# Kernel optimization log

Hardware: AMD Instinct MI355X
Metric: run time of the kernel (lower is better)

Reference implementation:

```python
import jax, jax.numpy as jnp
import numpy as np
import math

N_HEAD = 16
STRIDE = 128
C = 8


def _sparse_causal_mask(q_len, k_len):
    # Mirrors LingLongAttention._sparse_causal_mask (static, host-side numpy).
    cols = np.arange(k_len)
    rows = np.arange(k_len)[:, None]
    strided = (cols % STRIDE) >= (STRIDE - C)          # last C cols of each stride block
    local = (cols[None, :] // STRIDE) == (rows // STRIDE)  # same stride block as query
    causal = cols[None, :] <= rows
    layout = (strided[None, :] | local) & causal       # [k_len, k_len]
    return jnp.asarray(layout[k_len - q_len:])         # [q_len, k_len]


def setup_inputs() -> dict:
    key = jax.random.key(0)
    k1, k2, k3 = jax.random.split(key, 3)
    B, S, E = 2, 2048, 1024
    return {
        "hidden_states": jax.random.normal(k1, (B, S, E), dtype=jnp.float32),
        "W_attn": jax.random.normal(k2, (E, 3 * E), dtype=jnp.float32) * 0.02,
        "b_attn": jnp.zeros((3 * E,), dtype=jnp.float32),
        "W_proj": jax.random.normal(k3, (E, E), dtype=jnp.float32) * 0.02,
        "b_proj": jnp.zeros((E,), dtype=jnp.float32),
    }


def reference(hidden_states, W_attn, b_attn, W_proj, b_proj):
    B, S, E = hidden_states.shape
    H = N_HEAD
    D = E // H
    # Conv1D: x @ W + b, then split into q,k,v
    qkv = hidden_states @ W_attn + b_attn                 # [B,S,3E]
    q, k, v = jnp.split(qkv, 3, axis=-1)
    split = lambda t: t.reshape(B, S, H, D).transpose(0, 2, 1, 3)  # [B,H,S,D]
    q, k, v = split(q), split(k), split(v)
    scale = jnp.asarray(1.0 / math.sqrt(D), dtype=q.dtype)
    scores = jnp.einsum("bhqd,bhkd->bhqk", q, k) * scale  # [B,H,S,S]
    mask = _sparse_causal_mask(S, S)[None, None]          # [1,1,S,S]
    mask_value = jnp.asarray(jnp.finfo(scores.dtype).min, dtype=scores.dtype)
    scores = jnp.where(mask, scores, mask_value)
    attn = jax.nn.softmax(scores, axis=-1)
    out = jnp.einsum("bhqk,bhkd->bhqd", attn, v)          # [B,H,S,D]
    out = out.transpose(0, 2, 1, 3).reshape(B, S, E)      # merge heads
    return out @ W_proj + b_proj
```

## Files before the change

### kernel.cpp

```cpp
#include <hip/hip_runtime.h>
#include <hip/hip_bf16.h>
#include <stdint.h>

typedef unsigned short u16;
typedef uint32_t u32;
typedef short s16x8 __attribute__((ext_vector_type(8)));
typedef float f32x4 __attribute__((ext_vector_type(4)));

#define SDIM 2048
#define EDIM 1024

static __device__ __forceinline__ float b2f(u16 v) {
    union { float f; u32 u; } c; c.u = ((u32)v) << 16; return c.f;
}
static __device__ __forceinline__ u16 f2b(float f) {
    union { float f; u32 u; } c; c.f = f;
    u32 u = c.u;
    u32 r = (u + 0x7FFFu + ((u >> 16) & 1u)) >> 16;
    return (u16)r;
}
static __device__ __forceinline__ void gll16(const u16* g, u16* l) {
    __builtin_amdgcn_global_load_lds(
        (const __attribute__((address_space(1))) void*)g,
        (__attribute__((address_space(3))) void*)l, 16, 0, 0);
}

static __device__ __forceinline__ int sniff_bf16(const u16* __restrict__ x) {
    u16 v = x[(threadIdx.x & 63) * 2];
    int e = (v >> 7) & 0xFF;
    unsigned long long m = __ballot(e >= 90 && e <= 144);
    return __popcll(m) >= 48;
}

__global__ __launch_bounds__(256) void k_prep(
    const void* __restrict__ X, const void* __restrict__ Wa,
    const void* __restrict__ Wp, u16* __restrict__ Xb,
    u16* __restrict__ WtA, u16* __restrict__ WtP) {
    int f = sniff_bf16((const u16*)X);
    int z = blockIdx.z;
    int t = threadIdx.x;
    if (z == 2) {
        if (f) return;
        const float* s = (const float*)X;
        int bid = blockIdx.y * 48 + blockIdx.x;
        for (int c = bid; c < 2048; c += 768) {
            long i = ((long)c * 256 + t) * 8;
            u16 o[8];
            for (int j = 0; j < 8; ++j) o[j] = f2b(s[i + j]);
            *(uint4*)&Xb[i] = *(uint4*)o;
        }
        return;
    }
    if (z == 1 && blockIdx.x >= 16) return;
    const void* src = z ? Wp : Wa;
    u16* dst = z ? WtP : WtA;
    int Nsrc = z ? 1024 : 3072;
    int n0 = blockIdx.x * 64, k0 = blockIdx.y * 64;
    __shared__ u16 L[64 * 72];
    int r = t >> 2, c0 = (t & 3) * 16;
    u16 val[16];
    if (f) {
        const u16* s = (const u16*)src + (size_t)(k0 + r) * Nsrc + n0 + c0;
        *(uint4*)&val[0] = *(const uint4*)s;
        *(uint4*)&val[8] = *(const uint4*)(s + 8);
    } else {
        const float* s = (const float*)src + (size_t)(k0 + r) * Nsrc + n0 + c0;
        for (int j = 0; j < 16; ++j) val[j] = f2b(s[j]);
    }
    for (int j = 0; j < 16; ++j) L[(c0 + j) * 72 + r] = val[j];
    __syncthreads();
    uint4 o0 = *(const uint4*)&L[r * 72 + c0];
    uint4 o1 = *(const uint4*)&L[r * 72 + c0 + 8];
    u16* d = dst + (size_t)(n0 + r) * 1024 + k0 + c0;
    *(uint4*)d = o0;
    *(uint4*)(d + 8) = o1;
}

__global__ __launch_bounds__(256) void k_gemm1(
    const u16* __restrict__ Xraw, const u16* __restrict__ Xb,
    const u16* __restrict__ Bt, const void* __restrict__ bias,
    u16* __restrict__ C) {
    const int K = 1024;
    __shared__ u16 As[2][4096];
    __shared__ u16 Bs[2][4096];
    int f = sniff_bf16(Xraw);
    const u16* A = f ? Xraw : Xb;
    int t = threadIdx.x, wave = t >> 6, lane = t & 63;
    int m0 = blockIdx.y * 128, n0 = blockIdx.x * 128;
    int wm = (wave >> 1) * 64, wn = (wave & 1) * 64;
    int lm = lane & 15, lk = (lane >> 4) * 8;
    int sr = t >> 2, sc = (t & 3) * 8;
    const u16* Ap = A + (size_t)(m0 + sr) * K + sc;
    const u16* Bp = Bt + (size_t)(n0 + sr) * K + sc;
    int wo = wave * 512;

    f32x4 acc[4][4];
    f32x4 z = {0.f, 0.f, 0.f, 0.f};
    for (int mi = 0; mi < 4; ++mi)
        for (int ni = 0; ni < 4; ++ni) acc[mi][ni] = z;

    gll16(Ap, &As[0][wo]);
    gll16(Ap + (size_t)64 * K, &As[0][wo + 2048]);
    gll16(Bp, &Bs[0][wo]);
    gll16(Bp + (size_t)64 * K, &Bs[0][wo + 2048]);
    __syncthreads();

    for (int it = 0; it < 32; ++it) {
        int cur = it & 1;
        if (it < 31) {
            int kn = (it + 1) * 32;
            gll16(Ap + kn, &As[cur ^ 1][wo]);
            gll16(Ap + (size_t)64 * K + kn, &As[cur ^ 1][wo + 2048]);
            gll16(Bp + kn, &Bs[cur ^ 1][wo]);
            gll16(Bp + (size_t)64 * K + kn, &Bs[cur ^ 1][wo + 2048]);
        }
        s16x8 af[4], bfr[4];
        for (int mi = 0; mi < 4; ++mi)
            af[mi] = *(const s16x8*)&As[cur][(wm + mi * 16 + lm) * 32 + lk];
        for (int ni = 0; ni < 4; ++ni)
            bfr[ni] = *(const s16x8*)&Bs[cur][(wn + ni * 16 + lm) * 32 + lk];
        for (int mi = 0; mi < 4; ++mi)
            for (int ni = 0; ni < 4; ++ni)
                acc[mi][ni] = __builtin_amdgcn_mfma_f32_16x16x32_bf16(
                    af[mi], bfr[ni], acc[mi][ni], 0, 0, 0);
        __syncthreads();
    }

    int cn = lane & 15, cr = (lane >> 4) * 4;
    for (int ni = 0; ni < 4; ++ni) {
        int gn = n0 + wn + ni * 16 + cn;
        float bb = f ? b2f(((const u16*)bias)[gn]) : ((const float*)bias)[gn];
        int kind = gn >> 10, rem = gn & 1023;
        int h = rem >> 6, d = rem & 63;
        int hm = kind * 32 + h;
        for (int mi = 0; mi < 4; ++mi)
            for (int r = 0; r < 4; ++r) {
                int gm = m0 + wm + mi * 16 + cr + r;
                int b = gm >> 11, s = gm & 2047;
                size_t o = ((size_t)((hm + b * 16) * 2048 + s)) * 64 + d;
                C[o] = f2b(acc[mi][ni][r] + bb);
            }
    }
}

__global__ __launch_bounds__(256) void k_gemm2(
    const u16* __restrict__ Xraw, const u16* __restrict__ A,
    const u16* __restrict__ Bt, const void* __restrict__ bias,
    u16* __restrict__ Cb, float* __restrict__ Cf) {
    const int K = 1024, N = 1024;
    __shared__ u16 As[2][2048];
    __shared__ u16 Bs[2][4096];
    int f = sniff_bf16(Xraw);
    int t = threadIdx.x, wave = t >> 6, lane = t & 63;
    int m0 = blockIdx.y * 64, n0 = blockIdx.x * 128;
    int wm = (wave >> 1) * 32, wn = (wave & 1) * 64;
    int lm = lane & 15, lk = (lane >> 4) * 8;
    int sr = t >> 2, sc = (t & 3) * 8;
    const u16* Ap = A + (size_t)(m0 + sr) * K + sc;
    const u16* Bp = Bt + (size_t)(n0 + sr) * K + sc;
    int wo = wave * 512;

    f32x4 acc[2][4];
    f32x4 z = {0.f, 0.f, 0.f, 0.f};
    for (int mi = 0; mi < 2; ++mi)
        for (int ni = 0; ni < 4; ++ni) acc[mi][ni] = z;

    gll16(Ap, &As[0][wo]);
    gll16(Bp, &Bs[0][wo]);
    gll16(Bp + (size_t)64 * K, &Bs[0][wo + 2048]);
    __syncthreads();

    for (int it = 0; it < 32; ++it) {
        int cur = it & 1;
        if (it < 31) {
            int kn = (it + 1) * 32;
            gll16(Ap + kn, &As[cur ^ 1][wo]);
            gll16(Bp + kn, &Bs[cur ^ 1][wo]);
            gll16(Bp + (size_t)64 * K + kn, &Bs[cur ^ 1][wo + 2048]);
        }
        s16x8 af[2], bfr[4];
        for (int mi = 0; mi < 2; ++mi)
            af[mi] = *(const s16x8*)&As[cur][(wm + mi * 16 + lm) * 32 + lk];
        for (int ni = 0; ni < 4; ++ni)
            bfr[ni] = *(const s16x8*)&Bs[cur][(wn + ni * 16 + lm) * 32 + lk];
        for (int mi = 0; mi < 2; ++mi)
            for (int ni = 0; ni < 4; ++ni)
                acc[mi][ni] = __builtin_amdgcn_mfma_f32_16x16x32_bf16(
                    af[mi], bfr[ni], acc[mi][ni], 0, 0, 0);
        __syncthreads();
    }

    int store_f32 = (f == 0);
    int cn = lane & 15, cr = (lane >> 4) * 4;
    for (int ni = 0; ni < 4; ++ni) {
        int gn = n0 + wn + ni * 16 + cn;
        float bb = f ? b2f(((const u16*)bias)[gn]) : ((const float*)bias)[gn];
        for (int mi = 0; mi < 2; ++mi)
            for (int r = 0; r < 4; ++r) {
                int gm = m0 + wm + mi * 16 + cr + r;
                float v = acc[mi][ni][r] + bb;
                size_t o = (size_t)gm * N + gn;
                if (store_f32) Cf[o] = v;
                else           Cb[o] = f2b(v);
            }
    }
}

#define VP 264
#define PP 264
__global__ __launch_bounds__(256) void k_attn4(const u16* __restrict__ QKV,
                                               u16* __restrict__ AO) {
    int bx = blockIdx.x, h = blockIdx.y, b = blockIdx.z;
    int qb = bx >> 1, sb = bx & 1;
    int t = threadIdx.x, lane = t & 63, wave = t >> 6;
    int lm = lane & 15, q4 = lane >> 4;
    int nstr = qb << 3;
    int nk = nstr + (sb << 6) + 64;
    int r0 = (qb << 7) + (sb << 6);

    __shared__ char smem[79872];
    u16* Vts = (u16*)smem;
    u16* Qs  = (u16*)(smem + 33792);
    u16* Ks  = (u16*)(smem + 33792 + 9216);
    u16* Ps  = (u16*)(smem + 33792);

    int hm = b * 16 + h;
    const u16* qp = QKV + ((size_t)hm * 2048 + r0) * 64;
    const u16* kp = QKV + ((size_t)(32 + hm) * 2048) * 64;
    const u16* vp = QKV + ((size_t)(64 + hm) * 2048) * 64;

    for (int c = t; c < 512; c += 256) {
        int r = c >> 3, d0 = (c & 7) << 3;
        *(uint4*)&Qs[r * 72 + d0] = *(const uint4*)(qp + c * 8);
    }
    uint4 zz = {0u, 0u, 0u, 0u};
    for (int c = t; c < 2048; c += 256) {
        int i = c >> 3, d0 = (c & 7) << 3;
        uint4 kv = zz;
        if (i < nk) {
            int key = (i < nstr) ? (((i >> 3) << 7) + 120 + (i & 7))
                                 : ((qb << 7) + (i - nstr));
            kv = *(const uint4*)(kp + key * 64 + d0);
        }
        *(uint4*)&Ks[i * 72 + d0] = kv;
    }
    {
        int i0 = (t & 31) * 8, d0 = (t >> 5) * 8;
        u16 m8[8][8];
        for (int r = 0; r < 8; ++r) {
            int i = i0 + r;
            uint4 vv = zz;
            if (i < nk) {
                int key = (i < nstr) ? (((i >> 3) << 7) + 120 + (i & 7))
                                     : ((qb << 7) + (i - nstr));
                vv = *(const uint4*)(vp + key * 64 + d0);
            }
            *(uint4*)m8[r] = vv;
        }
        for (int j = 0; j < 8; ++j) {
            u16 o[8];
            for (int r = 0; r < 8; ++r) o[r] = m8[r][j];
            *(uint4*)&Vts[(d0 + j) * VP + i0] = *(uint4*)o;
        }
    }
    __syncthreads();

    f32x4 acc[16];
    f32x4 z4 = {0.f, 0.f, 0.f, 0.f};
    for (int ni = 0; ni < 16; ++ni) acc[ni] = z4;
    s16x8 af0 = *(const s16x8*)&Qs[(wave * 16 + lm) * 72 + q4 * 8];
    s16x8 af1 = *(const s16x8*)&Qs[(wave * 16 + lm) * 72 + 32 + q4 * 8];
    for (int ni = 0; ni < 16; ++ni) {
        s16x8 bf0 = *(const s16x8*)&Ks[(ni * 16 + lm) * 72 + q4 * 8];
        s16x8 bf1 = *(const s16x8*)&Ks[(ni * 16 + lm) * 72 + 32 + q4 * 8];
        acc[ni] = __builtin_amdgcn_mfma_f32_16x16x32_bf16(af0, bf0, acc[ni], 0, 0, 0);
        acc[ni] = __builtin_amdgcn_mfma_f32_16x16x32_bf16(af1, bf1, acc[ni], 0, 0, 0);
    }
    __syncthreads();

    float mx[4] = {-3e38f, -3e38f, -3e38f, -3e38f};
    for (int ni = 0; ni < 16; ++ni) {
        int i = ni * 16 + lm;
        for (int reg = 0; reg < 4; ++reg) {
            int rl = (sb << 6) + wave * 16 + q4 * 4 + reg;
            bool valid = (i < nstr) || ((i - nstr) <= rl);
            float v = valid ? acc[ni][reg] * 0.125f : -3e38f;
            acc[ni][reg] = v;
            mx[reg] = fmaxf(mx[reg], v);
        }
    }
    for (int reg = 0; reg < 4; ++reg)
        for (int off = 1; off < 16; off <<= 1)
            mx[reg] = fmaxf(mx[reg], __shfl_xor(mx[reg], off, 64));
    float sm[4] = {0.f, 0.f, 0.f, 0.f};
    for (int ni = 0; ni < 16; ++ni)
        for (int reg = 0; reg < 4; ++reg) {
            float e = __expf(acc[ni][reg] - mx[reg]);
            acc[ni][reg] = e;
            sm[reg] += e;
        }
    for (int reg = 0; reg < 4; ++reg)
        for (int off = 1; off < 16; off <<= 1)
            sm[reg] += __shfl_xor(sm[reg], off, 64);
    float inv[4];
    for (int reg = 0; reg < 4; ++reg) inv[reg] = 1.f / sm[reg];

    for (int ni = 0; ni < 16; ++ni) {
        int i = ni * 16 + lm;
        for (int reg = 0; reg < 4; ++reg)
            Ps[(wave * 16 + q4 * 4 + reg) * PP + i] = f2b(acc[ni][reg]);
    }
    __syncthreads();

    f32x4 acc2[4];
    for (int ni2 = 0; ni2 < 4; ++ni2) acc2[ni2] = z4;
    for (int k0 = 0; k0 < 256; k0 += 32) {
        s16x8 pf = *(const s16x8*)&Ps[(wave * 16 + lm) * PP + k0 + q4 * 8];
        for (int ni2 = 0; ni2 < 4; ++ni2) {
            s16x8 vf = *(const s16x8*)&Vts[(ni2 * 16 + lm) * VP + k0 + q4 * 8];
            acc2[ni2] = __builtin_amdgcn_mfma_f32_16x16x32_bf16(pf, vf, acc2[ni2], 0, 0, 0);
        }
    }
    int srow = r0 + wave * 16 + q4 * 4;
    for (int ni2 = 0; ni2 < 4; ++ni2)
        for (int reg = 0; reg < 4; ++reg) {
            size_t o = ((size_t)(b * SDIM + srow + reg)) * EDIM + h * 64 + ni2 * 16 + lm;
            AO[o] = f2b(acc2[ni2][reg] * inv[reg]);
        }
}

extern "C" void kernel_launch(void* const* d_in, const int* in_sizes, int n_in,
                              void* d_out, int out_size, void* d_ws, size_t ws_size,
                              hipStream_t stream) {
    const void* X  = d_in[0];
    const void* Wa = d_in[1];
    const void* ba = d_in[2];
    const void* Wp = d_in[3];
    const void* bp = d_in[4];

    char* w = (char*)d_ws;
    u16* Xb   = (u16*)(w);
    u16* WtA  = (u16*)(w + 8388608);
    u16* WtP  = (u16*)(w + 14680064);
    u16* QKVh = (u16*)(w + 16777216);
    u16* AO   = (u16*)(w + 41943040);

    k_prep<<<dim3(48, 16, 3), 256, 0, stream>>>(X, Wa, Wp, Xb, WtA, WtP);
    k_gemm1<<<dim3(24, 32), 256, 0, stream>>>((const u16*)X, Xb, WtA, ba, QKVh);
    k_attn4<<<dim3(32, 16, 2), 256, 0, stream>>>(QKVh, AO);
    k_gemm2<<<dim3(8, 64), 256, 0, stream>>>((const u16*)X, AO, WtP, bp,
                                             (u16*)d_out, (float*)d_out);
}
```

Measured before the change: 169.4 us.

## Deepen GEMM LDS pipeline with split-K stages and fine-grained vmcnt waits

Both projection GEMMs now keep two K=64 buffers, each split into two 32-wide chunks, and issue the next tile's loads chunk by chunk. Full __syncthreads barriers are replaced by explicit s_waitcnt vmcnt(N) plus s_barrier, so only the oldest chunk has to land before it is used. This keeps more global-to-LDS loads in flight across the MFMA work, at the cost of doubled LDS use and hand-tuned wait counts. The last iteration issues a redundant wraparound prefetch that is drained with vmcnt(0).

```diff
diff --git a/kernel.cpp b/kernel.cpp
--- a/kernel.cpp
+++ b/kernel.cpp
@@ -76,55 +76,68 @@
     *(uint4*)(d + 8) = o1;
 }
 
+#define G1_STAGE(bufi, kc, kt) do {                                          \
+    gll16(Ab + (kt) * 64 + (kc) * 32,             &As[bufi][kc][wave * 512]); \
+    gll16(Ab + (kt) * 64 + (kc) * 32 + 64 * 1024, &As[bufi][kc][wave * 512 + 2048]); \
+    gll16(Bb + (kt) * 64 + (kc) * 32,             &Bs[bufi][kc][wave * 512]); \
+    gll16(Bb + (kt) * 64 + (kc) * 32 + 64 * 1024, &Bs[bufi][kc][wave * 512 + 2048]); \
+} while (0)
+
 __global__ __launch_bounds__(256) void k_gemm1(
     const u16* __restrict__ Xraw, const u16* __restrict__ Xb,
     const u16* __restrict__ Bt, const void* __restrict__ bias,
     u16* __restrict__ C) {
     const int K = 1024;
-    __shared__ u16 As[2][4096];
-    __shared__ u16 Bs[2][4096];
+    __shared__ u16 As[2][2][4096];
+    __shared__ u16 Bs[2][2][4096];
     int f = sniff_bf16(Xraw);
     const u16* A = f ? Xraw : Xb;
     int t = threadIdx.x, wave = t >> 6, lane = t & 63;
     int m0 = blockIdx.y * 128, n0 = blockIdx.x * 128;
     int wm = (wave >> 1) * 64, wn = (wave & 1) * 64;
-    int lm = lane & 15, lk = (lane >> 4) * 8;
-    int sr = t >> 2, sc = (t & 3) * 8;
-    const u16* Ap = A + (size_t)(m0 + sr) * K + sc;
-    const u16* Bp = Bt + (size_t)(n0 + sr) * K + sc;
-    int wo = wave * 512;
+    int lm = lane & 15, q4 = lane >> 4;
+    int srow = wave * 16 + (lane >> 2), scol = (lane & 3) * 8;
+    const u16* Ab = A  + (size_t)(m0 + srow) * K + scol;
+    const u16* Bb = Bt + (size_t)(n0 + srow) * K + scol;
 
     f32x4 acc[4][4];
     f32x4 z = {0.f, 0.f, 0.f, 0.f};
     for (int mi = 0; mi < 4; ++mi)
         for (int ni = 0; ni < 4; ++ni) acc[mi][ni] = z;
 
-    gll16(Ap, &As[0][wo]);
-    gll16(Ap + (size_t)64 * K, &As[0][wo + 2048]);
-    gll16(Bp, &Bs[0][wo]);
-    gll16(Bp + (size_t)64 * K, &Bs[0][wo + 2048]);
-    __syncthreads();
-
-    for (int it = 0; it < 32; ++it) {
-        int cur = it & 1;
-        if (it < 31) {
-            int kn = (it + 1) * 32;
-            gll16(Ap + kn, &As[cur ^ 1][wo]);
-            gll16(Ap + (size_t)64 * K + kn, &As[cur ^ 1][wo + 2048]);
-            gll16(Bp + kn, &Bs[cur ^ 1][wo]);
-            gll16(Bp + (size_t)64 * K + kn, &Bs[cur ^ 1][wo + 2048]);
-        }
-        s16x8 af[4], bfr[4];
-        for (int mi = 0; mi < 4; ++mi)
-            af[mi] = *(const s16x8*)&As[cur][(wm + mi * 16 + lm) * 32 + lk];
-        for (int ni = 0; ni < 4; ++ni)
-            bfr[ni] = *(const s16x8*)&Bs[cur][(wn + ni * 16 + lm) * 32 + lk];
-        for (int mi = 0; mi < 4; ++mi)
+    G1_STAGE(0, 0, 0);
+    G1_STAGE(0, 1, 0);
+
+    for (int it = 0; it < 16; ++it) {
+        int cur = it & 1, nb = cur ^ 1, nxt = (it + 1) & 15;
+        asm volatile("s_waitcnt vmcnt(4) lgkmcnt(0)\n\ts_barrier" ::: "memory");
+        G1_STAGE(nb, 0, nxt);
+        {
+            s16x8 af[4], bf[4];
+            for (int mi = 0; mi < 4; ++mi)
+                af[mi] = *(const s16x8*)&As[cur][0][(wm + mi * 16 + lm) * 32 + q4 * 8];
             for (int ni = 0; ni < 4; ++ni)
-                acc[mi][ni] = __builtin_amdgcn_mfma_f32_16x16x32_bf16(
-                    af[mi], bfr[ni], acc[mi][ni], 0, 0, 0);
-        __syncthreads();
-    }
+                bf[ni] = *(const s16x8*)&Bs[cur][0][(wn + ni * 16 + lm) * 32 + q4 * 8];
+            for (int mi = 0; mi < 4; ++mi)
+                for (int ni = 0; ni < 4; ++ni)
+                    acc[mi][ni] = __builtin_amdgcn_mfma_f32_16x16x32_bf16(
+                        af[mi], bf[ni], acc[mi][ni], 0, 0, 0);
+        }
+        asm volatile("s_waitcnt vmcnt(4) lgkmcnt(0)\n\ts_barrier" ::: "memory");
+        G1_STAGE(nb, 1, nxt);
+        {
+            s16x8 af[4], bf[4];
+            for (int mi = 0; mi < 4; ++mi)
+                af[mi] = *(const s16x8*)&As[cur][1][(wm + mi * 16 + lm) * 32 + q4 * 8];
+            for (int ni = 0; ni < 4; ++ni)
+                bf[ni] = *(const s16x8*)&Bs[cur][1][(wn + ni * 16 + lm) * 32 + q4 * 8];
+            for (int mi = 0; mi < 4; ++mi)
+                for (int ni = 0; ni < 4; ++ni)
+                    acc[mi][ni] = __builtin_amdgcn_mfma_f32_16x16x32_bf16(
+                        af[mi], bf[ni], acc[mi][ni], 0, 0, 0);
+        }
+    }
+    asm volatile("s_waitcnt vmcnt(0)" ::: "memory");
 
     int cn = lane & 15, cr = (lane >> 4) * 4;
     for (int ni = 0; ni < 4; ++ni) {
@@ -143,52 +156,66 @@
     }
 }
 
+#define G2_STAGE(bufi, kc, kt) do {                                          \
+    gll16(Ab + (kt) * 64 + (kc) * 32,             &As[bufi][kc][wave * 512]); \
+    gll16(Bb + (kt) * 64 + (kc) * 32,             &Bs[bufi][kc][wave * 512]); \
+    gll16(Bb + (kt) * 64 + (kc) * 32 + 64 * 1024, &Bs[bufi][kc][wave * 512 + 2048]); \
+} while (0)
+
 __global__ __launch_bounds__(256) void k_gemm2(
     const u16* __restrict__ Xraw, const u16* __restrict__ A,
     const u16* __restrict__ Bt, const void* __restrict__ bias,
     u16* __restrict__ Cb, float* __restrict__ Cf) {
     const int K = 1024, N = 1024;
-    __shared__ u16 As[2][2048];
-    __shared__ u16 Bs[2][4096];
+    __shared__ u16 As[2][2][2048];
+    __shared__ u16 Bs[2][2][4096];
     int f = sniff_bf16(Xraw);
     int t = threadIdx.x, wave = t >> 6, lane = t & 63;
     int m0 = blockIdx.y * 64, n0 = blockIdx.x * 128;
     int wm = (wave >> 1) * 32, wn = (wave & 1) * 64;
-    int lm = lane & 15, lk = (lane >> 4) * 8;
-    int sr = t >> 2, sc = (t & 3) * 8;
-    const u16* Ap = A + (size_t)(m0 + sr) * K + sc;
-    const u16* Bp = Bt + (size_t)(n0 + sr) * K + sc;
-    int wo = wave * 512;
+    int lm = lane & 15, q4 = lane >> 4;
+    int srow = wave * 16 + (lane >> 2), scol = (lane & 3) * 8;
+    const u16* Ab = A  + (size_t)(m0 + srow) * K + scol;
+    const u16* Bb = Bt + (size_t)(n0 + srow) * K + scol;
 
     f32x4 acc[2][4];
     f32x4 z = {0.f, 0.f, 0.f, 0.f};
     for (int mi = 0; mi < 2; ++mi)
         for (int ni = 0; ni < 4; ++ni) acc[mi][ni] = z;
 
-    gll16(Ap, &As[0][wo]);
-    gll16(Bp, &Bs[0][wo]);
-    gll16(Bp + (size_t)64 * K, &Bs[0][wo + 2048]);
-    __syncthreads();
-
-    for (int it = 0; it < 32; ++it) {
-        int cur = it & 1;
-        if (it < 31) {
-            int kn = (it + 1) * 32;
-            gll16(Ap + kn, &As[cur ^ 1][wo]);
-            gll16(Bp + kn, &Bs[cur ^ 1][wo]);
-            gll16(Bp + (size_t)64 * K + kn, &Bs[cur ^ 1][wo + 2048]);
-        }
-        s16x8 af[2], bfr[4];
-        for (int mi = 0; mi < 2; ++mi)
-            af[mi] = *(const s16x8*)&As[cur][(wm + mi * 16 + lm) * 32 + lk];
-        for (int ni = 0; ni < 4; ++ni)
-            bfr[ni] = *(const s16x8*)&Bs[cur][(wn + ni * 16 + lm) * 32 + lk];
-        for (int mi = 0; mi < 2; ++mi)
+    G2_STAGE(0, 0, 0);
+    G2_STAGE(0, 1, 0);
+
+    for (int it = 0; it < 16; ++it) {
+        int cur = it & 1, nb = cur ^ 1, nxt = (it + 1) & 15;
+        asm volatile("s_waitcnt vmcnt(3) lgkmcnt(0)\n\ts_barrier" ::: "memory");
+        G2_STAGE(nb, 0, nxt);
+        {
+            s16x8 af[2], bf[4];
+            for (int mi = 0; mi < 2; ++mi)
+                af[mi] = *(const s16x8*)&As[cur][0][(wm + mi * 16 + lm) * 32 + q4 * 8];
             for (int ni = 0; ni < 4; ++ni)
-                acc[mi][ni] = __builtin_amdgcn_mfma_f32_16x16x32_bf16(
-                    af[mi], bfr[ni], acc[mi][ni], 0, 0, 0);
-        __syncthreads();
-    }
+                bf[ni] = *(const s16x8*)&Bs[cur][0][(wn + ni * 16 + lm) * 32 + q4 * 8];
+            for (int mi = 0; mi < 2; ++mi)
+                for (int ni = 0; ni < 4; ++ni)
+                    acc[mi][ni] = __builtin_amdgcn_mfma_f32_16x16x32_bf16(
+                        af[mi], bf[ni], acc[mi][ni], 0, 0, 0);
+        }
+        asm volatile("s_waitcnt vmcnt(3) lgkmcnt(0)\n\ts_barrier" ::: "memory");
+        G2_STAGE(nb, 1, nxt);
+        {
+            s16x8 af[2], bf[4];
+            for (int mi = 0; mi < 2; ++mi)
+                af[mi] = *(const s16x8*)&As[cur][1][(wm + mi * 16 + lm) * 32 + q4 * 8];
+            for (int ni = 0; ni < 4; ++ni)
+                bf[ni] = *(const s16x8*)&Bs[cur][1][(wn + ni * 16 + lm) * 32 + q4 * 8];
+            for (int mi = 0; mi < 2; ++mi)
+                for (int ni = 0; ni < 4; ++ni)
+                    acc[mi][ni] = __builtin_amdgcn_mfma_f32_16x16x32_bf16(
+                        af[mi], bf[ni], acc[mi][ni], 0, 0, 0);
+        }
+    }
+    asm volatile("s_waitcnt vmcnt(0)" ::: "memory");
 
     int store_f32 = (f == 0);
     int cn = lane & 15, cr = (lane >> 4) * 4;
```

Result: slower. 184.0 us (+8.6%).

## Triple-buffer LDS in projection GEMMs with one barrier per K-step

Applied to the files above, without the earlier changes.

Both projection GEMM kernels move from double-buffered to triple-buffered LDS tiles. Async global-to-LDS loads are issued two K-steps ahead, and each iteration has a single waitcnt+barrier at its top instead of a trailing __syncthreads. This hides more global-load latency and removes one barrier per step. It costs 50% more LDS, which may lower occupancy, and the last iterations issue wasted wrap-around loads.

```diff
diff --git a/kernel.cpp b/kernel.cpp
--- a/kernel.cpp
+++ b/kernel.cpp
@@ -81,8 +81,8 @@
     const u16* __restrict__ Bt, const void* __restrict__ bias,
     u16* __restrict__ C) {
     const int K = 1024;
-    __shared__ u16 As[2][4096];
-    __shared__ u16 Bs[2][4096];
+    __shared__ u16 As[3][4096];
+    __shared__ u16 Bs[3][4096];
     int f = sniff_bf16(Xraw);
     const u16* A = f ? Xraw : Xb;
     int t = threadIdx.x, wave = t >> 6, lane = t & 63;
@@ -103,28 +103,36 @@
     gll16(Ap + (size_t)64 * K, &As[0][wo + 2048]);
     gll16(Bp, &Bs[0][wo]);
     gll16(Bp + (size_t)64 * K, &Bs[0][wo + 2048]);
-    __syncthreads();
+    gll16(Ap + 32, &As[1][wo]);
+    gll16(Ap + (size_t)64 * K + 32, &As[1][wo + 2048]);
+    gll16(Bp + 32, &Bs[1][wo]);
+    gll16(Bp + (size_t)64 * K + 32, &Bs[1][wo + 2048]);
+
+    u16 *Ac = &As[0][0], *An = &As[1][0], *At = &As[2][0];
+    u16 *Bc = &Bs[0][0], *Bn = &Bs[1][0], *Btg = &Bs[2][0];
 
     for (int it = 0; it < 32; ++it) {
-        int cur = it & 1;
-        if (it < 31) {
-            int kn = (it + 1) * 32;
-            gll16(Ap + kn, &As[cur ^ 1][wo]);
-            gll16(Ap + (size_t)64 * K + kn, &As[cur ^ 1][wo + 2048]);
-            gll16(Bp + kn, &Bs[cur ^ 1][wo]);
-            gll16(Bp + (size_t)64 * K + kn, &Bs[cur ^ 1][wo + 2048]);
-        }
+        asm volatile("s_waitcnt vmcnt(4)\n\ts_barrier" ::: "memory");
+        int kn = ((it + 2) & 31) * 32;
+        gll16(Ap + kn, At + wo);
+        gll16(Ap + (size_t)64 * K + kn, At + wo + 2048);
+        gll16(Bp + kn, Btg + wo);
+        gll16(Bp + (size_t)64 * K + kn, Btg + wo + 2048);
+
         s16x8 af[4], bfr[4];
         for (int mi = 0; mi < 4; ++mi)
-            af[mi] = *(const s16x8*)&As[cur][(wm + mi * 16 + lm) * 32 + lk];
+            af[mi] = *(const s16x8*)&Ac[(wm + mi * 16 + lm) * 32 + lk];
         for (int ni = 0; ni < 4; ++ni)
-            bfr[ni] = *(const s16x8*)&Bs[cur][(wn + ni * 16 + lm) * 32 + lk];
+            bfr[ni] = *(const s16x8*)&Bc[(wn + ni * 16 + lm) * 32 + lk];
         for (int mi = 0; mi < 4; ++mi)
             for (int ni = 0; ni < 4; ++ni)
                 acc[mi][ni] = __builtin_amdgcn_mfma_f32_16x16x32_bf16(
                     af[mi], bfr[ni], acc[mi][ni], 0, 0, 0);
-        __syncthreads();
-    }
+
+        u16* tp = Ac; Ac = An; An = At; At = tp;
+        tp = Bc; Bc = Bn; Bn = Btg; Btg = tp;
+    }
+    asm volatile("s_waitcnt vmcnt(0)" ::: "memory");
 
     int cn = lane & 15, cr = (lane >> 4) * 4;
     for (int ni = 0; ni < 4; ++ni) {
@@ -148,8 +156,8 @@
     const u16* __restrict__ Bt, const void* __restrict__ bias,
     u16* __restrict__ Cb, float* __restrict__ Cf) {
     const int K = 1024, N = 1024;
-    __shared__ u16 As[2][2048];
-    __shared__ u16 Bs[2][4096];
+    __shared__ u16 As[3][2048];
+    __shared__ u16 Bs[3][4096];
     int f = sniff_bf16(Xraw);
     int t = threadIdx.x, wave = t >> 6, lane = t & 63;
     int m0 = blockIdx.y * 64, n0 = blockIdx.x * 128;
@@ -168,27 +176,34 @@
     gll16(Ap, &As[0][wo]);
     gll16(Bp, &Bs[0][wo]);
     gll16(Bp + (size_t)64 * K, &Bs[0][wo + 2048]);
-    __syncthreads();
+    gll16(Ap + 32, &As[1][wo]);
+    gll16(Bp + 32, &Bs[1][wo]);
+    gll16(Bp + (size_t)64 * K + 32, &Bs[1][wo + 2048]);
+
+    u16 *Ac = &As[0][0], *An = &As[1][0], *At = &As[2][0];
+    u16 *Bc = &Bs[0][0], *Bn = &Bs[1][0], *Btg = &Bs[2][0];
 
     for (int it = 0; it < 32; ++it) {
-        int cur = it & 1;
-        if (it < 31) {
-            int kn = (it + 1) * 32;
-            gll16(Ap + kn, &As[cur ^ 1][wo]);
-            gll16(Bp + kn, &Bs[cur ^ 1][wo]);
-            gll16(Bp + (size_t)64 * K + kn, &Bs[cur ^ 1][wo + 2048]);
-        }
+        asm volatile("s_waitcnt vmcnt(3)\n\ts_barrier" ::: "memory");
+        int kn = ((it + 2) & 31) * 32;
+        gll16(Ap + kn, At + wo);
+        gll16(Bp + kn, Btg + wo);
+        gll16(Bp + (size_t)64 * K + kn, Btg + wo + 2048);
+
         s16x8 af[2], bfr[4];
         for (int mi = 0; mi < 2; ++mi)
-            af[mi] = *(const s16x8*)&As[cur][(wm + mi * 16 + lm) * 32 + lk];
+            af[mi] = *(const s16x8*)&Ac[(wm + mi * 16 + lm) * 32 + lk];
         for (int ni = 0; ni < 4; ++ni)
-            bfr[ni] = *(const s16x8*)&Bs[cur][(wn + ni * 16 + lm) * 32 + lk];
+            bfr[ni] = *(const s16x8*)&Bc[(wn + ni * 16 + lm) * 32 + lk];
         for (int mi = 0; mi < 2; ++mi)
             for (int ni = 0; ni < 4; ++ni)
                 acc[mi][ni] = __builtin_amdgcn_mfma_f32_16x16x32_bf16(
                     af[mi], bfr[ni], acc[mi][ni], 0, 0, 0);
-        __syncthreads();
-    }
+
+        u16* tp = Ac; Ac = An; An = At; At = tp;
+        tp = Bc; Bc = Bn; Bn = Btg; Btg = tp;
+    }
+    asm volatile("s_waitcnt vmcnt(0)" ::: "memory");
 
     int store_f32 = (f == 0);
     int cn = lane & 15, cr = (lane >> 4) * 4;
```

Result: faster. 163.2 us (-3.7%).
